# Kernel tuning notes

Measured on AMD Instinct MI355X. Metric: run time of the kernel, lower is better.

The kernel has to match this reference:

```python
import jax, jax.numpy as jnp
import numpy as np

N_BOXES = 1_000_000
EPS = 1e-6


def box2corners(box):
    """(..., 5) [x,y,w,h,angle] -> (..., 4, 2) corners (mmcv box2corners)."""
    x, y, w, h, a = (box[..., i] for i in range(5))
    dx = jnp.asarray([0.5, -0.5, -0.5, 0.5], box.dtype) * w[..., None]  # (...,4)
    dy = jnp.asarray([0.5, 0.5, -0.5, -0.5], box.dtype) * h[..., None]
    cos, sin = jnp.cos(a)[..., None], jnp.sin(a)[..., None]
    cx = dx * cos - dy * sin + x[..., None]
    cy = dx * sin + dy * cos + y[..., None]
    return jnp.stack([cx, cy], axis=-1)


def box_intersection(c1, c2):
    """All 4x4 edge-pair segment intersections. c1,c2: (N,4,2).
    Returns pts (N,4,4,2), mask (N,4,4)."""
    roll = jnp.array([1, 2, 3, 0])
    line1 = jnp.concatenate([c1, c1[:, roll, :]], axis=-1)  # (N,4,4): x1,y1,x2,y2
    line2 = jnp.concatenate([c2, c2[:, roll, :]], axis=-1)
    l1 = line1[:, :, None, :]  # (N,4,1,4)
    l2 = line2[:, None, :, :]  # (N,1,4,4)
    x1, y1, x2, y2 = l1[..., 0], l1[..., 1], l1[..., 2], l1[..., 3]
    x3, y3, x4, y4 = l2[..., 0], l2[..., 1], l2[..., 2], l2[..., 3]
    num = (y4 - y3) * (x2 - x1) - (x4 - x3) * (y2 - y1)
    den_t = (x4 - x3) * (y1 - y3) - (y4 - y3) * (x1 - x3)
    safe = jnp.where(num == 0.0, 1.0, num)
    t = jnp.where(num == 0.0, -1.0, den_t / safe)
    mask_t = (t > 0) & (t < 1)
    den_u = (x2 - x1) * (y1 - y3) - (y2 - y1) * (x1 - x3)
    u = jnp.where(num == 0.0, -1.0, -den_u / safe)
    mask_u = (u > 0) & (u < 1)
    mask = mask_t & mask_u
    t2 = den_t / (num + 1e-8)
    pts = jnp.stack([x1 + t2 * (x2 - x1), y1 + t2 * (y2 - y1)], axis=-1)
    pts = pts * mask[..., None].astype(pts.dtype)
    return pts, mask


def box1_in_box2(c1, c2):
    """Which corners of c1 lie inside box c2. (N,4,2)x(N,4,2)->(N,4) bool."""
    a = c2[:, 0:1, :]
    b = c2[:, 1:2, :]
    d = c2[:, 3:4, :]
    ab, ad, am = b - a, d - a, c1 - a
    pab = jnp.sum(ab * am, -1) / jnp.sum(ab * ab, -1)
    pad_ = jnp.sum(ad * am, -1) / jnp.sum(ad * ad, -1)
    e = 1e-6
    return (pab > -e) & (pab < 1 + e) & (pad_ > -e) & (pad_ < 1 + e)


def intersection_area(c1, c2):
    """Differentiable rotated-box intersection area via convex polygon clipping."""
    inter_pts, inter_mask = box_intersection(c1, c2)
    m1 = box1_in_box2(c1, c2)
    m2 = box1_in_box2(c2, c1)
    n = c1.shape[0]
    verts = jnp.concatenate([c1, c2, inter_pts.reshape(n, 16, 2)], axis=1)  # (N,24,2)
    mask = jnp.concatenate([m1, m2, inter_mask.reshape(n, 16)], axis=1)     # (N,24)
    k = jnp.sum(mask, axis=-1)  # num valid vertices per box
    mf = mask.astype(verts.dtype)
    mean = jnp.sum(verts * mf[..., None], axis=1, keepdims=True) / \
        jnp.maximum(k, 1).astype(verts.dtype)[:, None, None]
    vn = verts - mean
    # sort valid vertices counterclockwise by angle around centroid; invalid last
    ang = jnp.where(mask, jnp.arctan2(vn[..., 1], vn[..., 0]), 1e9)
    order = jnp.argsort(ang, axis=-1)
    vs = jnp.take_along_axis(verts, order[..., None], axis=1)  # (N,24,2)
    idx = jnp.arange(24)
    nxt = jnp.where(idx[None, :] + 1 < k[:, None], idx[None, :] + 1, 0)
    v_next = jnp.take_along_axis(vs, nxt[..., None], axis=1)
    cross = vs[..., 0] * v_next[..., 1] - vs[..., 1] * v_next[..., 0]
    valid = idx[None, :] < k[:, None]
    return jnp.abs(jnp.sum(jnp.where(valid, cross, 0.0), axis=-1)) * 0.5


def fpdiou_loss(pred, target):
    c1 = box2corners(pred)
    c2 = box2corners(target)
    inter = intersection_area(c1, c2)
    area1 = pred[:, 2] * pred[:, 3]
    area2 = target[:, 2] * target[:, 3]
    iou = inter / (area1 + area2 - inter)
    iou = jnp.maximum(iou, EPS)
    # corner-distance term (detached in original via .detach().cpu().numpy())
    p = jax.lax.stop_gradient(c1)
    g = jax.lax.stop_gradient(c2)
    ps = jnp.take_along_axis(p, jnp.argsort(p[..., 0], axis=-1)[..., None], axis=1)
    gs = jnp.take_along_axis(g, jnp.argsort(g[..., 0], axis=-1)[..., None], axis=1)
    d = 2.0 * (gs[:, 0, 0] - ps[:, 0, 0]) ** 2 \
        + (ps[:, 1, 0] - gs[:, 1, 0]) ** 2 + (ps[:, 1, 1] - gs[:, 1, 1]) ** 2 \
        + (ps[:, 2, 0] - gs[:, 2, 0]) ** 2 + (ps[:, 2, 1] - gs[:, 2, 1]) ** 2 \
        + (ps[:, 3, 0] - gs[:, 3, 0]) ** 2 + (ps[:, 3, 1] - gs[:, 3, 1]) ** 2
    res = d / (4.0 * 1024.0 ** 2)
    loss = 1.0 - iou + res  # mode='linear'
    return jnp.mean(loss)   # reduction='mean', loss_weight=1.0


def setup_inputs() -> dict:
    key = jax.random.key(0)
    k1, k2, k3, k4 = jax.random.split(key, 4)
    xy = jax.random.uniform(k1, (N_BOXES, 2), minval=0.0, maxval=1024.0)
    wh = jax.random.uniform(k2, (N_BOXES, 2), minval=8.0, maxval=96.0)
    ang = jax.random.uniform(k3, (N_BOXES, 1), minval=-np.pi / 2, maxval=np.pi / 2)
    pred = jnp.concatenate([xy, wh, ang], axis=-1).astype(jnp.float32)
    scale = jnp.asarray([4.0, 4.0, 3.0, 3.0, 0.1], jnp.float32)
    target = pred + jax.random.normal(k4, (N_BOXES, 5), jnp.float32) * scale
    target = target.at[:, 2:4].set(jnp.maximum(target[:, 2:4], 4.0))
    return {"pred": pred, "target": target}


def reference(pred, target):
    return fpdiou_loss(pred, target)
```

## Files before the change

kernel.cpp:

```cpp
#include <hip/hip_runtime.h>

#define BS 256
#define NS 24

__device__ __forceinline__ float rcpf(float x) { return __builtin_amdgcn_rcpf(x); }

#define CSWAPK(A, B) do {                                         \
    const unsigned ka_ = key[A], kb_ = key[B];                    \
    key[A] = ka_ < kb_ ? ka_ : kb_;                               \
    key[B] = ka_ < kb_ ? kb_ : ka_;                               \
} while (0)

#define CSW2(x, y, I, J) do {                                     \
    const bool sw_ = (x[J] < x[I]);                               \
    const float xi_ = x[I], xj_ = x[J], yi_ = y[I], yj_ = y[J];   \
    x[I] = sw_ ? xj_ : xi_;  x[J] = sw_ ? xi_ : xj_;              \
    y[I] = sw_ ? yj_ : yi_;  y[J] = sw_ ? yi_ : yj_;              \
} while (0)

__global__ __launch_bounds__(BS, 4)
void fpdiou_kernel(const float* __restrict__ pred, const float* __restrict__ tgt,
                   float* __restrict__ out, int n, float inv_n)
{
    __shared__ unsigned s_p[NS * BS];
    __shared__ float s_red[BS / 64];

    const int tid = threadIdx.x;
    const int i = blockIdx.x * BS + tid;
    float loss = 0.f;

    if (i < n) {
        const float* pp = pred + (size_t)i * 5;
        const float* gg = tgt  + (size_t)i * 5;
        const float p0 = pp[0], p1 = pp[1], pw = pp[2], ph = pp[3], pa = pp[4];
        const float g0 = gg[0], g1 = gg[1], gw = gg[2], gh = gg[3], ga = gg[4];

        const float s1 = __sinf(pa), co1 = __cosf(pa);
        const float s2 = __sinf(ga), co2 = __cosf(ga);

        const float DX[4] = {0.5f, -0.5f, -0.5f, 0.5f};
        const float DY[4] = {0.5f,  0.5f, -0.5f, -0.5f};
        float c1x[4], c1y[4], c2x[4], c2y[4];
#pragma unroll
        for (int q = 0; q < 4; q++) {
            float dx = DX[q] * pw, dy = DY[q] * ph;
            c1x[q] = dx * co1 - dy * s1 + p0;
            c1y[q] = dx * s1 + dy * co1 + p1;
            dx = DX[q] * gw; dy = DY[q] * gh;
            c2x[q] = dx * co2 - dy * s2 + g0;
            c2y[q] = dx * s2 + dy * co2 + g1;
        }

        const float SCL = 128.f;

        float res;
        {
            float px_[4] = {c1x[0], c1x[1], c1x[2], c1x[3]};
            float py_[4] = {c1y[0], c1y[1], c1y[2], c1y[3]};
            float gx_[4] = {c2x[0], c2x[1], c2x[2], c2x[3]};
            float gy_[4] = {c2y[0], c2y[1], c2y[2], c2y[3]};
            CSW2(px_, py_, 0, 1); CSW2(px_, py_, 2, 3);
            CSW2(px_, py_, 0, 2); CSW2(px_, py_, 1, 3); CSW2(px_, py_, 1, 2);
            CSW2(gx_, gy_, 0, 1); CSW2(gx_, gy_, 2, 3);
            CSW2(gx_, gy_, 0, 2); CSW2(gx_, gy_, 1, 3); CSW2(gx_, gy_, 1, 2);
            const float d0 = gx_[0] - px_[0];
            float d = 2.f * d0 * d0;
#pragma unroll
            for (int q = 1; q < 4; q++) {
                const float dxq = px_[q] - gx_[q];
                const float dyq = py_[q] - gy_[q];
                d += dxq * dxq + dyq * dyq;
            }
            res = d * (1.f / 4194304.f);
        }

        unsigned vm = 0;
        float sx = 0.f, sy = 0.f;
        int k = 0;
        const float e = 1e-6f;

        {
            const float ax = c2x[0], ay = c2y[0];
            const float abx = c2x[1] - ax, aby = c2y[1] - ay;
            const float adx = c2x[3] - ax, ady = c2y[3] - ay;
            const float dab = abx * abx + aby * aby;
            const float dad = adx * adx + ady * ady;
            const float lo_ab = -e * dab, hi_ab = (1.f + e) * dab;
            const float lo_ad = -e * dad, hi_ad = (1.f + e) * dad;
#pragma unroll
            for (int q = 0; q < 4; q++) {
                const float amx = c1x[q] - ax, amy = c1y[q] - ay;
                const float dot_ab = abx * amx + aby * amy;
                const float dot_ad = adx * amx + ady * amy;
                const bool m = (dot_ab > lo_ab) & (dot_ab < hi_ab)
                             & (dot_ad > lo_ad) & (dot_ad < hi_ad);
                const int xi = (int)rintf((c1x[q] - p0) * SCL);
                const int yi = (int)rintf((c1y[q] - p1) * SCL);
                s_p[q * BS + tid] = ((unsigned)yi << 16) | ((unsigned)xi & 0xFFFFu);
                if (m) { vm |= 1u << q; sx += c1x[q]; sy += c1y[q]; k++; }
            }
        }
        {
            const float ax = c1x[0], ay = c1y[0];
            const float abx = c1x[1] - ax, aby = c1y[1] - ay;
            const float adx = c1x[3] - ax, ady = c1y[3] - ay;
            const float dab = abx * abx + aby * aby;
            const float dad = adx * adx + ady * ady;
            const float lo_ab = -e * dab, hi_ab = (1.f + e) * dab;
            const float lo_ad = -e * dad, hi_ad = (1.f + e) * dad;
#pragma unroll
            for (int q = 0; q < 4; q++) {
                const float amx = c2x[q] - ax, amy = c2y[q] - ay;
                const float dot_ab = abx * amx + aby * amy;
                const float dot_ad = adx * amx + ady * amy;
                const bool m = (dot_ab > lo_ab) & (dot_ab < hi_ab)
                             & (dot_ad > lo_ad) & (dot_ad < hi_ad);
                const int xi = (int)rintf((c2x[q] - p0) * SCL);
                const int yi = (int)rintf((c2y[q] - p1) * SCL);
                s_p[(4 + q) * BS + tid] = ((unsigned)yi << 16) | ((unsigned)xi & 0xFFFFu);
                if (m) { vm |= 1u << (4 + q); sx += c2x[q]; sy += c2y[q]; k++; }
            }
        }
        float iix[16], iiy[16];
#pragma unroll
        for (int a = 0; a < 4; a++) {
            const float x1 = c1x[a], y1 = c1y[a];
            const float ex = c1x[(a + 1) & 3] - x1, ey = c1y[(a + 1) & 3] - y1;
#pragma unroll
            for (int b = 0; b < 4; b++) {
                const float x3 = c2x[b], y3 = c2y[b];
                const float fx = c2x[(b + 1) & 3] - x3, fy = c2y[(b + 1) & 3] - y3;
                const float num = fy * ex - fx * ey;
                const float dx13 = x1 - x3, dy13 = y1 - y3;
                const float den_t = fx * dy13 - fy * dx13;
                const float den_u = ex * dy13 - ey * dx13;
                const bool m = (den_t * num > 0.f) & (fabsf(den_t) < fabsf(num))
                             & (den_u * num < 0.f) & (fabsf(den_u) < fabsf(num));
                const float t2 = den_t * rcpf(num + 1e-8f);
                const float ix = fmaf(t2, ex, x1), iy = fmaf(t2, ey, y1);
                const int s = 8 + a * 4 + b;
                iix[a * 4 + b] = ix; iiy[a * 4 + b] = iy;
                const int xi = (int)rintf((ix - p0) * SCL);
                const int yi = (int)rintf((iy - p1) * SCL);
                s_p[s * BS + tid] = ((unsigned)yi << 16) | ((unsigned)xi & 0xFFFFu);
                if (m) { vm |= 1u << s; sx += ix; sy += iy; k++; }
            }
        }

        const float kf = (float)(k > 0 ? k : 1);
        const float mx = sx / kf, my = sy / kf;
        unsigned key[NS];
#pragma unroll
        for (int s = 0; s < NS; s++) {
            const float vx = (s < 4) ? c1x[s] : (s < 8) ? c2x[s - 4] : iix[s - 8];
            const float vy = (s < 4) ? c1y[s] : (s < 8) ? c2y[s - 4] : iiy[s - 8];
            const float dx = vx - mx, dy = vy - my;
            const float sa = fabsf(dx) + fabsf(dy);
            float ang = copysignf(1.f - dx * rcpf(sa), dy);
            ang = (sa == 0.f) ? 0.f : ang;
            ang = ((vm >> s) & 1u) ? ang : 1e9f;
            unsigned bb = __float_as_uint(ang);
            bb ^= (unsigned)((int)bb >> 31) | 0x80000000u;
            key[s] = (bb & 0xFFFFFFE0u) | (unsigned)s;
        }

        CSWAPK(0,16); CSWAPK(1,17); CSWAPK(2,18); CSWAPK(3,19);
        CSWAPK(4,20); CSWAPK(5,21); CSWAPK(6,22); CSWAPK(7,23);
        CSWAPK(0,8);  CSWAPK(1,9);  CSWAPK(2,10); CSWAPK(3,11);
        CSWAPK(4,12); CSWAPK(5,13); CSWAPK(6,14); CSWAPK(7,15);
        CSWAPK(8,16); CSWAPK(9,17); CSWAPK(10,18); CSWAPK(11,19);
        CSWAPK(12,20); CSWAPK(13,21); CSWAPK(14,22); CSWAPK(15,23);
        CSWAPK(0,4);  CSWAPK(1,5);  CSWAPK(2,6);  CSWAPK(3,7);
        CSWAPK(8,12); CSWAPK(9,13); CSWAPK(10,14); CSWAPK(11,15);
        CSWAPK(16,20); CSWAPK(17,21); CSWAPK(18,22); CSWAPK(19,23);
        CSWAPK(4,16); CSWAPK(5,17); CSWAPK(6,18); CSWAPK(7,19);
        CSWAPK(4,8);  CSWAPK(5,9);  CSWAPK(6,10); CSWAPK(7,11);
        CSWAPK(12,16); CSWAPK(13,17); CSWAPK(14,18); CSWAPK(15,19);
        CSWAPK(0,2);  CSWAPK(1,3);  CSWAPK(4,6);  CSWAPK(5,7);
        CSWAPK(8,10); CSWAPK(9,11); CSWAPK(12,14); CSWAPK(13,15);
        CSWAPK(16,18); CSWAPK(17,19); CSWAPK(20,22); CSWAPK(21,23);
        CSWAPK(2,16); CSWAPK(3,17); CSWAPK(6,20); CSWAPK(7,21);
        CSWAPK(2,8);  CSWAPK(3,9);  CSWAPK(6,12); CSWAPK(7,13);
        CSWAPK(10,16); CSWAPK(11,17); CSWAPK(14,20); CSWAPK(15,21);
        CSWAPK(2,4);  CSWAPK(3,5);  CSWAPK(6,8);  CSWAPK(7,9);
        CSWAPK(10,12); CSWAPK(11,13); CSWAPK(14,16); CSWAPK(15,17);
        CSWAPK(18,20); CSWAPK(19,21);
        CSWAPK(0,1);  CSWAPK(2,3);  CSWAPK(4,5);  CSWAPK(6,7);
        CSWAPK(8,9);  CSWAPK(10,11); CSWAPK(12,13); CSWAPK(14,15);
        CSWAPK(16,17); CSWAPK(18,19); CSWAPK(20,21); CSWAPK(22,23);
        CSWAPK(1,16); CSWAPK(3,18); CSWAPK(5,20); CSWAPK(7,22);
        CSWAPK(1,8);  CSWAPK(3,10); CSWAPK(5,12); CSWAPK(7,14);
        CSWAPK(9,16); CSWAPK(11,18); CSWAPK(13,20); CSWAPK(15,22);
        CSWAPK(1,4);  CSWAPK(3,6);  CSWAPK(5,8);  CSWAPK(7,10);
        CSWAPK(9,12); CSWAPK(11,14); CSWAPK(13,16); CSWAPK(15,18);
        CSWAPK(17,20); CSWAPK(19,22);
        CSWAPK(1,2);  CSWAPK(3,4);  CSWAPK(5,6);  CSWAPK(7,8);
        CSWAPK(9,10); CSWAPK(11,12); CSWAPK(13,14); CSWAPK(15,16);
        CSWAPK(17,18); CSWAPK(19,20); CSWAPK(21,22);

        unsigned wv[NS];
#pragma unroll
        for (int j = 0; j < NS; j++)
            wv[j] = s_p[(key[j] & 31u) * BS + tid];
        float X[NS], Y[NS];
#pragma unroll
        for (int j = 0; j < NS; j++) {
            X[j] = (float)((int)(wv[j] << 16) >> 16);
            Y[j] = (float)((int)wv[j] >> 16);
        }
        float cr0 = 0.f, cr1 = 0.f, cr2 = 0.f;
#pragma unroll
        for (int j = 0; j + 1 < NS; j++) {
            const float t = (j + 1 < k) ? (X[j] * Y[j + 1] - Y[j] * X[j + 1]) : 0.f;
            if ((j % 3) == 0) cr0 += t; else if ((j % 3) == 1) cr1 += t; else cr2 += t;
        }
        float xk = 0.f, yk = 0.f;
#pragma unroll
        for (int j = 0; j < NS; j++) {
            const bool w = (j == k - 1);
            xk = w ? X[j] : xk;
            yk = w ? Y[j] : yk;
        }
        const float cr = (cr0 + cr1) + (cr2 + (xk * Y[0] - yk * X[0]));
        const float area = (k > 0) ? fabsf(cr) * (0.5f / 16384.f) : 0.f;

        const float a1 = pw * ph, a2 = gw * gh;
        float iou = area / (a1 + a2 - area);
        iou = fmaxf(iou, 1e-6f);
        loss = 1.f - iou + res;
    }

#pragma unroll
    for (int off = 32; off > 0; off >>= 1)
        loss += __shfl_down(loss, off, 64);
    if ((tid & 63) == 0) s_red[tid >> 6] = loss;
    __syncthreads();
    if (tid == 0) {
        float t = 0.f;
#pragma unroll
        for (int w = 0; w < BS / 64; w++) t += s_red[w];
        atomicAdd(out, t * inv_n);
    }
}

extern "C" void kernel_launch(void* const* d_in, const int* in_sizes, int n_in,
                              void* d_out, int out_size, void* d_ws, size_t ws_size,
                              hipStream_t stream)
{
    const float* pred = (const float*)d_in[0];
    const float* tgt  = (const float*)d_in[1];
    float* out = (float*)d_out;
    const int n = in_sizes[0] / 5;
    const int nblk = (n + BS - 1) / BS;

    hipMemsetAsync(out, 0, sizeof(float), stream);
    fpdiou_kernel<<<nblk, BS, 0, stream>>>(pred, tgt, out, n, 1.f / (float)n);
}
```

Measured before the change: 127.1 us.

## Compute polygon clipping in pred box local frame with axis-aligned edges

Moves the intersection geometry into the predicted box's rotated, scaled frame, where box1 becomes axis-aligned. Inside tests and edge intersections then reduce to simple comparisons and one-axis solves, and box1 corner keys become constants. The shoelace sum now pads unused slots with the first vertex instead of using per-index predicates and a separate closing term. The count comes from popc, and mean and angle use rcp and fma. The risks are small numerical differences from the frame change and truncating casts, plus slightly changed epsilon semantics.

```diff
diff --git a/kernel.cpp b/kernel.cpp
--- a/kernel.cpp
+++ b/kernel.cpp
@@ -38,27 +38,20 @@
         const float s1 = __sinf(pa), co1 = __cosf(pa);
         const float s2 = __sinf(ga), co2 = __cosf(ga);
 
-        const float DX[4] = {0.5f, -0.5f, -0.5f, 0.5f};
-        const float DY[4] = {0.5f,  0.5f, -0.5f, -0.5f};
-        float c1x[4], c1y[4], c2x[4], c2y[4];
-#pragma unroll
-        for (int q = 0; q < 4; q++) {
-            float dx = DX[q] * pw, dy = DY[q] * ph;
-            c1x[q] = dx * co1 - dy * s1 + p0;
-            c1y[q] = dx * s1 + dy * co1 + p1;
-            dx = DX[q] * gw; dy = DY[q] * gh;
-            c2x[q] = dx * co2 - dy * s2 + g0;
-            c2y[q] = dx * s2 + dy * co2 + g1;
-        }
-
-        const float SCL = 128.f;
-
         float res;
         {
-            float px_[4] = {c1x[0], c1x[1], c1x[2], c1x[3]};
-            float py_[4] = {c1y[0], c1y[1], c1y[2], c1y[3]};
-            float gx_[4] = {c2x[0], c2x[1], c2x[2], c2x[3]};
-            float gy_[4] = {c2y[0], c2y[1], c2y[2], c2y[3]};
+            const float DX[4] = {0.5f, -0.5f, -0.5f, 0.5f};
+            const float DY[4] = {0.5f,  0.5f, -0.5f, -0.5f};
+            float px_[4], py_[4], gx_[4], gy_[4];
+#pragma unroll
+            for (int q = 0; q < 4; q++) {
+                float dx = DX[q] * pw, dy = DY[q] * ph;
+                px_[q] = dx * co1 - dy * s1 + p0;
+                py_[q] = dx * s1 + dy * co1 + p1;
+                dx = DX[q] * gw; dy = DY[q] * gh;
+                gx_[q] = dx * co2 - dy * s2 + g0;
+                gy_[q] = dx * s2 + dy * co2 + g1;
+            }
             CSW2(px_, py_, 0, 1); CSW2(px_, py_, 2, 3);
             CSW2(px_, py_, 0, 2); CSW2(px_, py_, 1, 3); CSW2(px_, py_, 1, 2);
             CSW2(gx_, gy_, 0, 1); CSW2(gx_, gy_, 2, 3);
@@ -74,91 +67,142 @@
             res = d * (1.f / 4194304.f);
         }
 
+        const float Ws = 64.f * pw, Hs = 64.f * ph;
+        const float W2s = 64.f * gw, H2s = 64.f * gh;
+        const float twoWs = 2.f * Ws, twoHs = 2.f * Hs;
+        const float mtwoWs = -twoWs, mtwoHs = -twoHs;
+        const float cD = co1 * co2 + s1 * s2;
+        const float sD = co1 * s2 - s1 * co2;
+        const float gx = g0 - p0, gy = g1 - p1;
+        const float u2x = (co1 * gx + s1 * gy) * 128.f;
+        const float u2y = (co1 * gy - s1 * gx) * 128.f;
+
+        float c2wx[4], c2wy[4];
+        const float SGX[4] = {1.f, -1.f, -1.f, 1.f};
+        const float SGY[4] = {1.f, 1.f, -1.f, -1.f};
+#pragma unroll
+        for (int q = 0; q < 4; q++) {
+            const float dqx = SGX[q] * W2s, dqy = SGY[q] * H2s;
+            c2wx[q] = cD * dqx - sD * dqy + u2x;
+            c2wy[q] = sD * dqx + cD * dqy + u2y;
+        }
+
+        const int iW = (int)Ws, iH = (int)Hs;
+        const unsigned loW  = (unsigned)iW & 0xFFFFu;
+        const unsigned loMW = (unsigned)(-iW) & 0xFFFFu;
+        const unsigned hiH  = (unsigned)iH << 16;
+        const unsigned hiMH = (unsigned)(-iH) << 16;
+
+        bool mv[NS];
         unsigned vm = 0;
         float sx = 0.f, sy = 0.f;
-        int k = 0;
         const float e = 1e-6f;
 
-        {
-            const float ax = c2x[0], ay = c2y[0];
-            const float abx = c2x[1] - ax, aby = c2y[1] - ay;
-            const float adx = c2x[3] - ax, ady = c2y[3] - ay;
-            const float dab = abx * abx + aby * aby;
-            const float dad = adx * adx + ady * ady;
-            const float lo_ab = -e * dab, hi_ab = (1.f + e) * dab;
-            const float lo_ad = -e * dad, hi_ad = (1.f + e) * dad;
-#pragma unroll
-            for (int q = 0; q < 4; q++) {
-                const float amx = c1x[q] - ax, amy = c1y[q] - ay;
-                const float dot_ab = abx * amx + aby * amy;
-                const float dot_ad = adx * amx + ady * amy;
-                const bool m = (dot_ab > lo_ab) & (dot_ab < hi_ab)
-                             & (dot_ad > lo_ad) & (dot_ad < hi_ad);
-                const int xi = (int)rintf((c1x[q] - p0) * SCL);
-                const int yi = (int)rintf((c1y[q] - p1) * SCL);
-                s_p[q * BS + tid] = ((unsigned)yi << 16) | ((unsigned)xi & 0xFFFFu);
-                if (m) { vm |= 1u << q; sx += c1x[q]; sy += c1y[q]; k++; }
-            }
-        }
-        {
-            const float ax = c1x[0], ay = c1y[0];
-            const float abx = c1x[1] - ax, aby = c1y[1] - ay;
-            const float adx = c1x[3] - ax, ady = c1y[3] - ay;
-            const float dab = abx * abx + aby * aby;
-            const float dad = adx * adx + ady * ady;
-            const float lo_ab = -e * dab, hi_ab = (1.f + e) * dab;
-            const float lo_ad = -e * dad, hi_ad = (1.f + e) * dad;
-#pragma unroll
-            for (int q = 0; q < 4; q++) {
-                const float amx = c2x[q] - ax, amy = c2y[q] - ay;
-                const float dot_ab = abx * amx + aby * amy;
-                const float dot_ad = adx * amx + ady * amy;
-                const bool m = (dot_ab > lo_ab) & (dot_ab < hi_ab)
-                             & (dot_ad > lo_ad) & (dot_ad < hi_ad);
-                const int xi = (int)rintf((c2x[q] - p0) * SCL);
-                const int yi = (int)rintf((c2y[q] - p1) * SCL);
-                s_p[(4 + q) * BS + tid] = ((unsigned)yi << 16) | ((unsigned)xi & 0xFFFFu);
-                if (m) { vm |= 1u << (4 + q); sx += c2x[q]; sy += c2y[q]; k++; }
-            }
-        }
+        const float W2t = W2s * (1.f + 2.f * e), H2t = H2s * (1.f + 2.f * e);
+        const float q1x[4] = {Ws, -Ws, -Ws, Ws};
+        const float q1y[4] = {Hs, Hs, -Hs, -Hs};
+        const unsigned q1p[4] = {hiH | loW, hiH | loMW, hiMH | loMW, hiMH | loW};
+#pragma unroll
+        for (int q = 0; q < 4; q++) {
+            const float tx = q1x[q] - u2x, ty = q1y[q] - u2y;
+            const float x2 = cD * tx + sD * ty;
+            const float y2 = cD * ty - sD * tx;
+            const bool m = (fabsf(x2) < W2t) & (fabsf(y2) < H2t);
+            s_p[q * BS + tid] = q1p[q];
+            mv[q] = m;
+            if (m) { vm |= 1u << q; sx += q1x[q]; sy += q1y[q]; }
+        }
+        const float Wt = Ws * (1.f + 2.f * e), Ht = Hs * (1.f + 2.f * e);
+#pragma unroll
+        for (int q = 0; q < 4; q++) {
+            const bool m = (fabsf(c2wx[q]) < Wt) & (fabsf(c2wy[q]) < Ht);
+            s_p[(4 + q) * BS + tid] = (((unsigned)(int)c2wy[q]) << 16)
+                                    | (((unsigned)(int)c2wx[q]) & 0xFFFFu);
+            mv[4 + q] = m;
+            if (m) { vm |= 1u << (4 + q); sx += c2wx[q]; sy += c2wy[q]; }
+        }
+
+        float fx[4], fy[4], afx[4], afy[4], thh[4], thv[4];
+#pragma unroll
+        for (int b = 0; b < 4; b++) {
+            const int bn = (b + 1) & 3;
+            fx[b] = c2wx[bn] - c2wx[b]; fy[b] = c2wy[bn] - c2wy[b];
+            afx[b] = fabsf(fx[b]); afy[b] = fabsf(fy[b]);
+            thh[b] = afy[b] * twoWs;
+            thv[b] = afx[b] * twoHs;
+        }
+
         float iix[16], iiy[16];
 #pragma unroll
-        for (int a = 0; a < 4; a++) {
-            const float x1 = c1x[a], y1 = c1y[a];
-            const float ex = c1x[(a + 1) & 3] - x1, ey = c1y[(a + 1) & 3] - y1;
-#pragma unroll
-            for (int b = 0; b < 4; b++) {
-                const float x3 = c2x[b], y3 = c2y[b];
-                const float fx = c2x[(b + 1) & 3] - x3, fy = c2y[(b + 1) & 3] - y3;
-                const float num = fy * ex - fx * ey;
-                const float dx13 = x1 - x3, dy13 = y1 - y3;
-                const float den_t = fx * dy13 - fy * dx13;
-                const float den_u = ex * dy13 - ey * dx13;
-                const bool m = (den_t * num > 0.f) & (fabsf(den_t) < fabsf(num))
-                             & (den_u * num < 0.f) & (fabsf(den_u) < fabsf(num));
-                const float t2 = den_t * rcpf(num + 1e-8f);
-                const float ix = fmaf(t2, ex, x1), iy = fmaf(t2, ey, y1);
-                const int s = 8 + a * 4 + b;
-                iix[a * 4 + b] = ix; iiy[a * 4 + b] = iy;
-                const int xi = (int)rintf((ix - p0) * SCL);
-                const int yi = (int)rintf((iy - p1) * SCL);
-                s_p[s * BS + tid] = ((unsigned)yi << 16) | ((unsigned)xi & 0xFFFFu);
-                if (m) { vm |= 1u << s; sx += ix; sy += iy; k++; }
-            }
-        }
-
+        for (int b = 0; b < 4; b++) {
+            const float dx13 = Ws - c2wx[b], dy13 = Hs - c2wy[b];
+            const float dent = fx[b] * dy13 - fy[b] * dx13;
+            const bool m = (dent * fy[b] < 0.f) & (fabsf(dent) < thh[b])
+                         & (fy[b] * dy13 < 0.f) & (fabsf(dy13) < afy[b]);
+            const float t2 = dent * rcpf(fy[b] * mtwoWs + 1e-8f);
+            const float ix = fmaf(t2, mtwoWs, Ws);
+            const int s = 8 + b;
+            s_p[s * BS + tid] = hiH | (((unsigned)(int)ix) & 0xFFFFu);
+            iix[b] = ix; iiy[b] = Hs;
+            mv[s] = m;
+            if (m) { vm |= 1u << s; sx += ix; sy += Hs; }
+        }
+#pragma unroll
+        for (int b = 0; b < 4; b++) {
+            const float dx13 = -Ws - c2wx[b], dy13 = Hs - c2wy[b];
+            const float dent = fx[b] * dy13 - fy[b] * dx13;
+            const bool m = (dent * fx[b] > 0.f) & (fabsf(dent) < thv[b])
+                         & (fx[b] * dx13 < 0.f) & (fabsf(dx13) < afx[b]);
+            const float t2 = dent * rcpf(fx[b] * twoHs + 1e-8f);
+            const float iy = fmaf(t2, mtwoHs, Hs);
+            const int s = 12 + b;
+            s_p[s * BS + tid] = (((unsigned)(int)iy) << 16) | loMW;
+            iix[4 + b] = -Ws; iiy[4 + b] = iy;
+            mv[s] = m;
+            if (m) { vm |= 1u << s; sx += -Ws; sy += iy; }
+        }
+#pragma unroll
+        for (int b = 0; b < 4; b++) {
+            const float dx13 = -Ws - c2wx[b], dy13 = -Hs - c2wy[b];
+            const float dent = fx[b] * dy13 - fy[b] * dx13;
+            const bool m = (dent * fy[b] > 0.f) & (fabsf(dent) < thh[b])
+                         & (fy[b] * dy13 < 0.f) & (fabsf(dy13) < afy[b]);
+            const float t2 = dent * rcpf(fy[b] * twoWs + 1e-8f);
+            const float ix = fmaf(t2, twoWs, -Ws);
+            const int s = 16 + b;
+            s_p[s * BS + tid] = hiMH | (((unsigned)(int)ix) & 0xFFFFu);
+            iix[8 + b] = ix; iiy[8 + b] = -Hs;
+            mv[s] = m;
+            if (m) { vm |= 1u << s; sx += ix; sy += -Hs; }
+        }
+#pragma unroll
+        for (int b = 0; b < 4; b++) {
+            const float dx13 = Ws - c2wx[b], dy13 = -Hs - c2wy[b];
+            const float dent = fx[b] * dy13 - fy[b] * dx13;
+            const bool m = (dent * fx[b] < 0.f) & (fabsf(dent) < thv[b])
+                         & (fx[b] * dx13 < 0.f) & (fabsf(dx13) < afx[b]);
+            const float t2 = dent * rcpf(fx[b] * mtwoHs + 1e-8f);
+            const float iy = fmaf(t2, twoHs, -Hs);
+            const int s = 20 + b;
+            s_p[s * BS + tid] = (((unsigned)(int)iy) << 16) | loW;
+            iix[12 + b] = Ws; iiy[12 + b] = iy;
+            mv[s] = m;
+            if (m) { vm |= 1u << s; sx += Ws; sy += iy; }
+        }
+
+        const int k = __popc(vm);
         const float kf = (float)(k > 0 ? k : 1);
-        const float mx = sx / kf, my = sy / kf;
+        const float rk = rcpf(kf);
+        const float mx = sx * rk, my = sy * rk;
         unsigned key[NS];
 #pragma unroll
         for (int s = 0; s < NS; s++) {
-            const float vx = (s < 4) ? c1x[s] : (s < 8) ? c2x[s - 4] : iix[s - 8];
-            const float vy = (s < 4) ? c1y[s] : (s < 8) ? c2y[s - 4] : iiy[s - 8];
+            const float vx = (s < 4) ? q1x[s] : (s < 8) ? c2wx[s - 4] : iix[s - 8];
+            const float vy = (s < 4) ? q1y[s] : (s < 8) ? c2wy[s - 4] : iiy[s - 8];
             const float dx = vx - mx, dy = vy - my;
             const float sa = fabsf(dx) + fabsf(dy);
-            float ang = copysignf(1.f - dx * rcpf(sa), dy);
-            ang = (sa == 0.f) ? 0.f : ang;
-            ang = ((vm >> s) & 1u) ? ang : 1e9f;
+            float ang = copysignf(fmaf(-dx, rcpf(sa), 1.f), dy);
+            ang = mv[s] ? ang : 1e9f;
             unsigned bb = __float_as_uint(ang);
             bb ^= (unsigned)((int)bb >> 31) | 0x80000000u;
             key[s] = (bb & 0xFFFFFFE0u) | (unsigned)s;
@@ -202,6 +246,10 @@
 #pragma unroll
         for (int j = 0; j < NS; j++)
             wv[j] = s_p[(key[j] & 31u) * BS + tid];
+        const unsigned w0 = wv[0];
+#pragma unroll
+        for (int j = 1; j < NS; j++)
+            wv[j] = (j < k) ? wv[j] : w0;
         float X[NS], Y[NS];
 #pragma unroll
         for (int j = 0; j < NS; j++) {
@@ -210,19 +258,13 @@
         }
         float cr0 = 0.f, cr1 = 0.f, cr2 = 0.f;
 #pragma unroll
-        for (int j = 0; j + 1 < NS; j++) {
-            const float t = (j + 1 < k) ? (X[j] * Y[j + 1] - Y[j] * X[j + 1]) : 0.f;
+        for (int j = 0; j < NS; j++) {
+            const int jn = (j + 1 < NS) ? j + 1 : 0;
+            const float t = X[j] * Y[jn] - Y[j] * X[jn];
             if ((j % 3) == 0) cr0 += t; else if ((j % 3) == 1) cr1 += t; else cr2 += t;
         }
-        float xk = 0.f, yk = 0.f;
-#pragma unroll
-        for (int j = 0; j < NS; j++) {
-            const bool w = (j == k - 1);
-            xk = w ? X[j] : xk;
-            yk = w ? Y[j] : yk;
-        }
-        const float cr = (cr0 + cr1) + (cr2 + (xk * Y[0] - yk * X[0]));
-        const float area = (k > 0) ? fabsf(cr) * (0.5f / 16384.f) : 0.f;
+        const float cr = (cr0 + cr1) + cr2;
+        const float area = fabsf(cr) * (0.5f / 16384.f);
 
         const float a1 = pw * ph, a2 = gw * gh;
         float iou = area / (a1 + a2 - area);
```

Result: slower. 129.9 us (+2.2%).
